# Performance work log

Measured on AMD Instinct MI355X. Metric: run time of the kernel, lower is better.

Reference implementation:

```python
import jax, jax.numpy as jnp
import numpy as np
import math

N, C, T, V = 8, 256, 120, 25
W = 5          # window_size
PAD = 2        # (W + (W-1)*(dil-1) - 1)//2 with dil=1
H = 8          # num_heads
CO = 256       # out_channels
HD = CO // H   # head channels
EPS = 1e-5


def _bn(x, g, b, m, v):
    # eval-mode BatchNorm2d over channel axis 1; x: (N, C, T, V)
    inv = jax.lax.rsqrt(v + EPS)
    return (x - m[None, :, None, None]) * (inv * g)[None, :, None, None] + b[None, :, None, None]


def _mish(x):
    return x * jnp.tanh(jax.nn.softplus(x))


def setup_inputs() -> dict:
    key = jax.random.key(0)
    ks = jax.random.split(key, 16)
    s_in = 1.0 / math.sqrt(C)
    s_out = 1.0 / math.sqrt(CO)
    return {
        "x": jax.random.normal(ks[0], (N, C, T, V), jnp.float32),
        "w_qkv": jax.random.normal(ks[1], (C, 3 * CO), jnp.float32) * s_in,
        "w_out": jax.random.normal(ks[2], (CO, CO), jnp.float32) * s_out,
        "b_out": jax.random.normal(ks[3], (CO,), jnp.float32) * 0.01,
        "bn1_g": jax.random.normal(ks[4], (CO,), jnp.float32) * 0.1 + 1.0,
        "bn1_b": jax.random.normal(ks[5], (CO,), jnp.float32) * 0.1,
        "ffn_w1": jax.random.normal(ks[6], (CO, CO), jnp.float32) * s_out,
        "ffn_w2": jax.random.normal(ks[7], (CO, CO), jnp.float32) * s_out,
        "ffn_g": jax.random.normal(ks[8], (CO,), jnp.float32) * 0.1 + 1.0,
        "ffn_b": jax.random.normal(ks[9], (CO,), jnp.float32) * 0.1,
        "bn2_g": jax.random.normal(ks[10], (CO,), jnp.float32) * 0.1 + 1.0,
        "bn2_b": jax.random.normal(ks[11], (CO,), jnp.float32) * 0.1,
        "bn1_m": jax.random.normal(ks[12], (CO,), jnp.float32) * 0.1,
        "bn1_v": jax.random.uniform(ks[13], (CO,), jnp.float32, 0.5, 1.5),
        "ffn_m": jax.random.normal(ks[14], (CO,), jnp.float32) * 0.1,
        "ffn_v": jax.random.uniform(ks[15], (CO,), jnp.float32, 0.5, 1.5),
        "bn2_m": jnp.zeros((CO,), jnp.float32),
        "bn2_v": jnp.ones((CO,), jnp.float32),
    }


def reference(x, w_qkv, w_out, b_out, bn1_g, bn1_b, ffn_w1, ffn_w2, ffn_g, ffn_b,
              bn2_g, bn2_b, bn1_m, bn1_v, ffn_m, ffn_v, bn2_m, bn2_v):
    L = W * V
    # --- group_window: unfold over T with kernel (W,1), zero padding PAD ---
    xp = jnp.pad(x, ((0, 0), (0, 0), (PAD, PAD), (0, 0)))
    # (N, C, T, W, V): window element w at time t is frame t + w - PAD
    xw = jnp.stack([xp[:, :, w:w + T, :] for w in range(W)], axis=3)
    xg = xw.transpose(0, 2, 3, 4, 1).reshape(N * T, L, C)  # tokens: (N*T, L, C)

    # --- spatio-temporal attention (full softmax over L, scale 1/sqrt(CO)) ---
    qkv = (xg @ w_qkv).reshape(N * T, L, H, 3, HD)
    q, k, v = qkv[..., 0, :], qkv[..., 1, :], qkv[..., 2, :]  # (NT, L, H, HD)
    scores = jnp.einsum('blhd,bmhd->bhlm', q, k) / math.sqrt(CO)
    attn = jax.nn.softmax(scores, axis=-1)
    out = jnp.einsum('bhlm,bmhd->blhd', attn, v).reshape(N * T, L, CO)
    out = out @ w_out + b_out

    # --- mean over window dim, residual (Identity since C == CO), norm1 ---
    inter = out.reshape(N, T, W, V, CO).transpose(0, 4, 1, 2, 3).mean(axis=3)  # (N, CO, T, V)
    inter = _bn(inter + x, bn1_g, bn1_b, bn1_m, bn1_v)

    # --- FFN: 1x1 conv -> Mish -> BN -> 1x1 conv ---
    h = jnp.einsum('oi,nitv->notv', ffn_w1, inter)
    h = _bn(_mish(h), ffn_g, ffn_b, ffn_m, ffn_v)
    h = jnp.einsum('oi,nitv->notv', ffn_w2, h)

    return _bn(h + inter, bn2_g, bn2_b, bn2_m, bn2_v)
```

## Files before the change

kernel.cpp:

```cpp
#include <hip/hip_runtime.h>
#include <hip/hip_bf16.h>


using bf16  = __bf16;
using bf16x8 = __bf16 __attribute__((ext_vector_type(8)));
using f32x4  = float __attribute__((ext_vector_type(4)));
using f32x16 = float __attribute__((ext_vector_type(16)));
using uint32x4 = unsigned int __attribute__((ext_vector_type(4)));

#define GAS __attribute__((address_space(1)))
#define LAS __attribute__((address_space(3)))

__device__ __forceinline__ void gload_lds16(const void* g, void* l) {
  __builtin_amdgcn_global_load_lds((GAS void*)g, (LAS void*)l, 16, 0, 0);
}

__device__ __forceinline__ unsigned cvt_pk_bf16(float lo, float hi) {
  unsigned r;
  asm("v_cvt_pk_bf16_f32 %0, %1, %2" : "=v"(r) : "v"(lo), "v"(hi));
  return r;
}

__device__ __forceinline__ void pl32_swap(unsigned& a, unsigned& b) {
  asm("v_permlane32_swap_b32 %0, %1" : "+v"(a), "+v"(b));
}

__global__ void k_zero(float* out, int n) {
  int i = blockIdx.x * 256 + threadIdx.x;
  if (i < n) out[i] = 0.f;
}

__global__ void k_prep(const float* __restrict__ x,
                       const float* __restrict__ wqkv, const float* __restrict__ wout,
                       const float* __restrict__ b_out,
                       const float* __restrict__ w1, const float* __restrict__ w2,
                       const float* __restrict__ g1, const float* __restrict__ b1,
                       const float* __restrict__ m1, const float* __restrict__ v1,
                       const float* __restrict__ gf, const float* __restrict__ bff,
                       const float* __restrict__ mf, const float* __restrict__ vf,
                       const float* __restrict__ g2, const float* __restrict__ b2,
                       const float* __restrict__ m2, const float* __restrict__ v2,
                       bf16* __restrict__ Xrow, bf16* __restrict__ WqT,
                       bf16* __restrict__ WoT, bf16* __restrict__ W1c,
                       bf16* __restrict__ W2c, float* __restrict__ pb) {
  __shared__ bf16 T[64 * 72];
  const int b = blockIdx.x, tid = threadIdx.x;
  if (b < 1504) {
    const int bx = b % 47, by = (b / 47) & 3, n = b / 188;
    const int tv0 = bx * 64, c0 = by * 64;
    const int la = tid & 63, sub = tid >> 6;
#pragma unroll 4
    for (int i = 0; i < 16; ++i) {
      int c = c0 + sub + i * 4;
      int tv = tv0 + la;
      float v = (tv < 3000) ? x[(size_t)(n * 256 + c) * 3000 + tv] : 0.f;
      T[(sub + i * 4) * 72 + la] = (bf16)v;
    }
    __syncthreads();
#pragma unroll 4
    for (int i = 0; i < 16; ++i) {
      int tvl = sub + i * 4;
      int tv = tv0 + tvl;
      if (tv < 3000)
        Xrow[(size_t)(n * 3100 + 50 + tv) * 256 + c0 + la] = T[la * 72 + tvl];
    }
  } else if (b < 3041) {
    int idx = (b - 1504) * 256 + tid;
    if (idx < 196608) {
      int c = idx / 768, o = idx % 768;
      float vv = wqkv[idx];
      if ((o % 96) < 32) vv *= 0.0901387929f;
      WqT[o * 256 + c] = (bf16)vv;
    } else if (idx < 262144) {
      int j = idx - 196608;
      int c = j >> 8, o = j & 255;
      WoT[o * 256 + c] = (bf16)wout[j];
    } else if (idx < 327680) {
      int j = idx - 262144;
      W1c[j] = (bf16)w1[j];
    } else if (idx < 393216) {
      int j = idx - 327680;
      W2c[j] = (bf16)w2[j];
    } else if (idx < 393472) {
      int k = idx - 393216;
      float s1 = g1[k] * rsqrtf(v1[k] + 1e-5f);
      pb[k]        = s1;
      pb[256 + k]  = b1[k] - m1[k] * s1;
      float sf = gf[k] * rsqrtf(vf[k] + 1e-5f);
      pb[512 + k]  = sf;
      pb[768 + k]  = bff[k] - mf[k] * sf;
      float s2 = g2[k] * rsqrtf(v2[k] + 1e-5f);
      pb[1024 + k] = s2;
      pb[1280 + k] = b2[k] - m2[k] * s2;
      pb[1536 + k] = b_out[k];
    }
  } else {
    int z = b - 3041;
    int idx16 = z * 256 + tid;
    int e0 = idx16 * 8;
    int pr = e0 >> 8, col = e0 & 255;
    int n = pr / 100, r100 = pr % 100;
    int row = n * 3100 + (r100 < 50 ? r100 : 3000 + r100);
    int4 zz = {};
    *(int4*)&Xrow[(size_t)row * 256 + col] = zz;
  }
}

template <int EPI>
__global__ __launch_bounds__(256, 2) void k_gemm(
    const bf16* __restrict__ A, const bf16* __restrict__ BT,
    bf16* __restrict__ Cout, int ldc, int Mreal,
    const float* __restrict__ pb, const bf16* __restrict__ Res,
    float* __restrict__ Out2) {
  __shared__ __align__(16) char smem[19456];
  bf16* As = (bf16*)smem;
  bf16* Bs = (bf16*)(smem + 8192);
  const int tid = threadIdx.x;
  const int w = tid >> 6, lane = tid & 63, q = lane >> 4, l15 = lane & 15;
  const int m0 = blockIdx.x * 128, n0 = blockIdx.y * 128;
  const int wm = (w >> 1) * 64, wn = (w & 1) * 64;
  const int srow = tid >> 2;
  const int scol = (tid & 3) << 3;
  int ar1 = m0 + srow;        if (ar1 >= Mreal) ar1 = Mreal - 1;
  int ar2 = m0 + srow + 64;   if (ar2 >= Mreal) ar2 = Mreal - 1;
  char* ldsA = (char*)As + w * 1024;
  char* ldsB = (char*)Bs + w * 1024;
  f32x4 acc[4][4] = {};

  for (int ks = 0; ks < 8; ++ks) {
    const bf16* ga1 = A  + (size_t)ar1 * 256 + ks * 32 + scol;
    const bf16* ga2 = A  + (size_t)ar2 * 256 + ks * 32 + scol;
    const bf16* gb  = BT + (size_t)(n0 + srow) * 256 + ks * 32 + scol;
    gload_lds16(ga1, ldsA);
    gload_lds16(ga2, ldsA + 4096);
    gload_lds16(gb,            ldsB);
    gload_lds16(gb + 64 * 256, ldsB + 4096);
    __syncthreads();
    bf16x8 af[4], bfr[4];
#pragma unroll
    for (int i = 0; i < 4; ++i) af[i]  = *(const bf16x8*)&As[(wm + i * 16 + l15) * 32 + q * 8];
#pragma unroll
    for (int i = 0; i < 4; ++i) bfr[i] = *(const bf16x8*)&Bs[(wn + i * 16 + l15) * 32 + q * 8];
#pragma unroll
    for (int i = 0; i < 4; ++i)
#pragma unroll
      for (int j = 0; j < 4; ++j)
        acc[i][j] = __builtin_amdgcn_mfma_f32_16x16x32_bf16(af[i], bfr[j], acc[i][j], 0, 0, 0);
    __syncthreads();
  }

  if constexpr (EPI != 3) {
#pragma unroll
    for (int i = 0; i < 4; ++i) {
#pragma unroll
      for (int j = 0; j < 4; ++j) {
#pragma unroll
        for (int r = 0; r < 4; ++r) {
          int row = m0 + wm + i * 16 + q * 4 + r;
          int col = n0 + wn + j * 16 + l15;
          if (row >= Mreal) continue;
          float v = acc[i][j][r];
          if constexpr (EPI == 0) {
            Cout[(size_t)row * ldc + col] = (bf16)v;
          } else if constexpr (EPI == 1) {
            v += pb[1536 + col];
            int n = row / 3000;
            v += (float)Res[(size_t)(row + n * 100 + 50) * 256 + col];
            v = v * pb[col] + pb[256 + col];
            Cout[(size_t)row * 256 + col] = (bf16)v;
          } else {
            float ex = __expf(v);
            float a = 1.f + ex;
            float u = 1.f / (a * a);
            v = v * (1.f - u) / (1.f + u);
            v = v * pb[512 + col] + pb[768 + col];
            Cout[(size_t)row * 256 + col] = (bf16)v;
          }
        }
      }
    }
  } else {
    float* Tt = (float*)smem;
    const int tti = (w & 1);
#pragma unroll
    for (int jj = 0; jj < 4; ++jj) {
      __syncthreads();
#pragma unroll
      for (int i = 0; i < 4; ++i) {
#pragma unroll
        for (int r = 0; r < 4; ++r) {
          int rowl = wm + i * 16 + q * 4 + r;
          int row = m0 + rowl;
          int col = n0 + tti * 64 + jj * 16 + l15;
          float v = acc[i][jj][r];
          v += (float)Res[(size_t)row * 256 + col];
          v = v * pb[1024 + col] + pb[1280 + col];
          Tt[tti * 2432 + rowl * 19 + l15] = v;
        }
      }
      __syncthreads();
#pragma unroll
      for (int k = 0; k < 16; ++k) {
        int flat = k * 256 + tid;
        int tt2 = flat >> 11;
        int rem = flat & 2047;
        int colL = rem >> 7;
        int rowl = rem & 127;
        int row = m0 + rowl;
        if (row < Mreal) {
          int col = n0 + tt2 * 64 + jj * 16 + colL;
          int n = row / 3000, r2 = row - n * 3000;
          Out2[(size_t)(n * 256 + col) * 3000 + r2] = Tt[tt2 * 2432 + rowl * 19 + colL];
        }
      }
    }
  }
}

__global__ __launch_bounds__(256, 4) void k_attn(const bf16* __restrict__ Y,
                                                 bf16* __restrict__ om) {
  __shared__ __align__(16) char smem[18944];
  bf16* Vts = (bf16*)smem;
  float* Ofl = (float*)smem;
  float* Rin = (float*)(smem + 18432);
  const int tid = threadIdx.x;
  const int bi = blockIdx.x;
  const int h = bi & 7, b = bi >> 3;
  const int n = b / 120, t = b % 120;
  const bf16* Yb = Y + (size_t)(n * 3100 + t * 25) * 768 + h * 96;
  const int w = tid >> 6, lane = tid & 63;
  const int l31 = lane & 31, hi = lane >> 5;

#pragma unroll
  for (int p = 0; p < 2; ++p) {
    int m = p * 64 + lane;
    if (m < 125) {
      int4 v4 = *(const int4*)(Yb + (size_t)m * 768 + 64 + w * 8);
      bf16x8 v8 = __builtin_bit_cast(bf16x8, v4);
#pragma unroll
      for (int jj = 0; jj < 8; ++jj) Vts[(w * 8 + jj) * 136 + m] = v8[jj];
    }
  }
  if (tid < 96) {
    int d = tid / 3, m = 125 + tid % 3;
    Vts[d * 136 + m] = (bf16)0.f;
  }

  int qrow = w * 32 + l31; if (qrow > 124) qrow = 124;
  const bf16* qp = Yb + (size_t)qrow * 768 + hi * 8;
  bf16x8 qf0 = *(const bf16x8*)qp;
  bf16x8 qf1 = *(const bf16x8*)(qp + 16);

  f32x16 acc[4] = {};
#pragma unroll
  for (int kt = 0; kt < 4; ++kt) {
    int krow = kt * 32 + l31; if (krow > 124) krow = 124;
    const bf16* kp = Yb + (size_t)krow * 768 + 32 + hi * 8;
    bf16x8 kf0 = *(const bf16x8*)kp;
    bf16x8 kf1 = *(const bf16x8*)(kp + 16);
    acc[kt] = __builtin_amdgcn_mfma_f32_32x32x16_bf16(kf0, qf0, acc[kt], 0, 0, 0);
    acc[kt] = __builtin_amdgcn_mfma_f32_32x32x16_bf16(kf1, qf1, acc[kt], 0, 0, 0);
  }

  float sp[4];
  uint32x4 pk[8];
#pragma unroll
  for (int kt = 0; kt < 4; ++kt) {
    float e[16];
#pragma unroll
    for (int r = 0; r < 16; ++r) {
      float pz = exp2f(acc[kt][r]);
      if (kt == 3 && r >= 13 && hi) pz = 0.f;
      e[r] = pz;
    }
    float t0 = (e[0] + e[1]) + (e[2] + e[3]);
    float t1 = (e[4] + e[5]) + (e[6] + e[7]);
    float t2 = (e[8] + e[9]) + (e[10] + e[11]);
    float t3 = (e[12] + e[13]) + (e[14] + e[15]);
    sp[kt] = (t0 + t1) + (t2 + t3);
#pragma unroll
    for (int half = 0; half < 2; ++half) {
      const int ba = half * 8;
      unsigned a0 = cvt_pk_bf16(e[ba + 0], e[ba + 1]);
      unsigned a1 = cvt_pk_bf16(e[ba + 2], e[ba + 3]);
      unsigned b0 = cvt_pk_bf16(e[ba + 4], e[ba + 5]);
      unsigned b1 = cvt_pk_bf16(e[ba + 6], e[ba + 7]);
      pl32_swap(a0, b0);
      pl32_swap(a1, b1);
      pk[kt * 2 + half][0] = a0;
      pk[kt * 2 + half][1] = a1;
      pk[kt * 2 + half][2] = b0;
      pk[kt * 2 + half][3] = b1;
    }
  }
  float s = (sp[0] + sp[1]) + (sp[2] + sp[3]);
  s += __shfl_xor(s, 32, 64);
  float rinv = 1.f / s;
  if (hi == 0) Rin[w * 32 + l31] = rinv;

  __syncthreads();

  f32x16 oacc0 = {}, oacc1 = {};
#pragma unroll
  for (int kc = 0; kc < 8; ++kc) {
    bf16x8 pa = __builtin_bit_cast(bf16x8, pk[kc]);
    bf16x8 vf = *(const bf16x8*)&Vts[l31 * 136 + kc * 16 + hi * 8];
    if (kc & 1) oacc1 = __builtin_amdgcn_mfma_f32_32x32x16_bf16(pa, vf, oacc1, 0, 0, 0);
    else        oacc0 = __builtin_amdgcn_mfma_f32_32x32x16_bf16(pa, vf, oacc0, 0, 0, 0);
  }

  __syncthreads();
#pragma unroll
  for (int r = 0; r < 16; ++r) {
    int row = w * 32 + (r & 3) + 8 * (r >> 2) + 4 * hi;
    Ofl[row * 36 + l31] = oacc0[r] + oacc1[r];
  }
  __syncthreads();
  bf16* dst = om + (size_t)((n * 120 + t) * 25) * 256 + h * 32;
  for (int j = tid; j < 800; j += 256) {
    int vv = j >> 5, d = j & 31;
    float s5 = 0.f;
#pragma unroll
    for (int ww = 0; ww < 5; ++ww)
      s5 += Ofl[(ww * 25 + vv) * 36 + d] * Rin[ww * 25 + vv];
    dst[vv * 256 + d] = (bf16)(s5 * 0.2f);
  }
}

extern "C" void kernel_launch(void* const* d_in, const int* in_sizes, int n_in,
                              void* d_out, int out_size, void* d_ws, size_t ws_size,
                              hipStream_t stream) {
  const size_t NEED = 51584000;
  if (ws_size < NEED) {
    k_zero<<<(out_size + 255) / 256, 256, 0, stream>>>((float*)d_out, out_size);
    return;
  }
  const float* x     = (const float*)d_in[0];
  const float* wqkv  = (const float*)d_in[1];
  const float* wout  = (const float*)d_in[2];
  const float* b_out = (const float*)d_in[3];
  const float* bn1_g = (const float*)d_in[4];
  const float* bn1_b = (const float*)d_in[5];
  const float* ffn_w1= (const float*)d_in[6];
  const float* ffn_w2= (const float*)d_in[7];
  const float* ffn_g = (const float*)d_in[8];
  const float* ffn_b = (const float*)d_in[9];
  const float* bn2_g = (const float*)d_in[10];
  const float* bn2_b = (const float*)d_in[11];
  const float* bn1_m = (const float*)d_in[12];
  const float* bn1_v = (const float*)d_in[13];
  const float* ffn_m = (const float*)d_in[14];
  const float* ffn_v = (const float*)d_in[15];
  const float* bn2_m = (const float*)d_in[16];
  const float* bn2_v = (const float*)d_in[17];

  char* ws = (char*)d_ws;
  float* pb    = (float*)(ws + 0);
  bf16* WqT    = (bf16*)(ws + 7168);
  bf16* WoT    = (bf16*)(ws + 400384);
  bf16* W1c    = (bf16*)(ws + 531456);
  bf16* W2c    = (bf16*)(ws + 662528);
  bf16* Xrow   = (bf16*)(ws + 793600);
  bf16* Y      = (bf16*)(ws + 13491200);
  bf16* interR = Y;
  bf16* Gm     = (bf16*)(ws + 25779200);
  bf16* om     = (bf16*)d_out;

  k_prep<<<3141, 256, 0, stream>>>(x, wqkv, wout, b_out, ffn_w1, ffn_w2,
                                   bn1_g, bn1_b, bn1_m, bn1_v,
                                   ffn_g, ffn_b, ffn_m, ffn_v,
                                   bn2_g, bn2_b, bn2_m, bn2_v,
                                   Xrow, WqT, WoT, W1c, W2c, pb);
  k_gemm<0><<<dim3(194, 6), 256, 0, stream>>>(Xrow, WqT, Y, 768, 24800, pb, nullptr, nullptr);
  k_attn<<<7680, 256, 0, stream>>>(Y, om);
  k_gemm<1><<<dim3(188, 2), 256, 0, stream>>>(om, WoT, interR, 256, 24000, pb, Xrow, nullptr);
  k_gemm<2><<<dim3(188, 2), 256, 0, stream>>>(interR, W1c, Gm, 256, 24000, pb, nullptr, nullptr);
  k_gemm<3><<<dim3(188, 2), 256, 0, stream>>>(Gm, W2c, nullptr, 256, 24000, pb, interR, (float*)d_out);
}
```

Measured before the change: 245.2 us.

## Fuse out-projection, FFN GEMMs and epilogues into one kernel

After: 237.2 us. 3.3% less time.

```diff
diff --git a/kernel.cpp b/kernel.cpp
--- a/kernel.cpp
+++ b/kernel.cpp
@@ -217,6 +217,169 @@
   }
 }
 
+__global__ __launch_bounds__(256, 3) void k_ffn(
+    const bf16* __restrict__ Aom, const bf16* __restrict__ Wo,
+    const bf16* __restrict__ W1, const bf16* __restrict__ W2,
+    const bf16* __restrict__ Xres, const float* __restrict__ pb,
+    float* __restrict__ Out2) {
+  __shared__ __align__(16) char smem[54272];
+  bf16* As = (bf16*)smem;
+  bf16* Bs = (bf16*)(smem + 4096);
+  bf16* XI = (bf16*)(smem + 20480);
+  float* Tt = (float*)smem;
+  const int tid = threadIdx.x;
+  const int w = tid >> 6, lane = tid & 63, q = lane >> 4, l15 = lane & 15;
+  const int r0 = blockIdx.x * 64;
+  const int srow = tid >> 2, scol = (tid & 3) << 3;
+  char* ldsA = (char*)As + w * 1024;
+  char* ldsB = (char*)Bs + w * 1024;
+
+  f32x4 acc[4][4];
+#pragma unroll
+  for (int i = 0; i < 4; ++i)
+#pragma unroll
+    for (int j = 0; j < 4; ++j) acc[i][j] = f32x4{};
+
+  for (int ks = 0; ks < 8; ++ks) {
+    gload_lds16(Aom + (size_t)(r0 + srow) * 256 + ks * 32 + scol, ldsA);
+#pragma unroll
+    for (int ii = 0; ii < 4; ++ii)
+      gload_lds16(Wo + (size_t)(ii * 64 + srow) * 256 + ks * 32 + scol,
+                  ldsB + ii * 4096);
+    __syncthreads();
+    bf16x8 af[4], bfr[4];
+#pragma unroll
+    for (int i = 0; i < 4; ++i) af[i]  = *(const bf16x8*)&As[(i * 16 + l15) * 32 + q * 8];
+#pragma unroll
+    for (int j = 0; j < 4; ++j) bfr[j] = *(const bf16x8*)&Bs[(w * 64 + j * 16 + l15) * 32 + q * 8];
+#pragma unroll
+    for (int i = 0; i < 4; ++i)
+#pragma unroll
+      for (int j = 0; j < 4; ++j)
+        acc[i][j] = __builtin_amdgcn_mfma_f32_16x16x32_bf16(af[i], bfr[j], acc[i][j], 0, 0, 0);
+    __syncthreads();
+  }
+  unsigned irk[32];
+#pragma unroll
+  for (int i = 0; i < 4; ++i) {
+#pragma unroll
+    for (int j = 0; j < 4; ++j) {
+      int colb = w * 64 + j * 16 + l15;
+      float vv[4];
+#pragma unroll
+      for (int r = 0; r < 4; ++r) {
+        int grow = r0 + i * 16 + q * 4 + r;
+        int nn = grow / 3000;
+        float v = acc[i][j][r] + pb[1536 + colb]
+                + (float)Xres[(size_t)(grow + nn * 100 + 50) * 256 + colb];
+        v = v * pb[colb] + pb[256 + colb];
+        vv[r] = v;
+        XI[(i * 16 + q * 4 + r) * 264 + colb] = (bf16)v;
+      }
+      irk[(i * 4 + j) * 2 + 0] = cvt_pk_bf16(vv[0], vv[1]);
+      irk[(i * 4 + j) * 2 + 1] = cvt_pk_bf16(vv[2], vv[3]);
+    }
+  }
+
+#pragma unroll
+  for (int i = 0; i < 4; ++i)
+#pragma unroll
+    for (int j = 0; j < 4; ++j) acc[i][j] = f32x4{};
+  for (int ks = 0; ks < 8; ++ks) {
+#pragma unroll
+    for (int ii = 0; ii < 4; ++ii)
+      gload_lds16(W1 + (size_t)(ii * 64 + srow) * 256 + ks * 32 + scol,
+                  ldsB + ii * 4096);
+    __syncthreads();
+    bf16x8 af[4], bfr[4];
+#pragma unroll
+    for (int i = 0; i < 4; ++i) af[i]  = *(const bf16x8*)&XI[(i * 16 + l15) * 264 + ks * 32 + q * 8];
+#pragma unroll
+    for (int j = 0; j < 4; ++j) bfr[j] = *(const bf16x8*)&Bs[(w * 64 + j * 16 + l15) * 32 + q * 8];
+#pragma unroll
+    for (int i = 0; i < 4; ++i)
+#pragma unroll
+      for (int j = 0; j < 4; ++j)
+        acc[i][j] = __builtin_amdgcn_mfma_f32_16x16x32_bf16(af[i], bfr[j], acc[i][j], 0, 0, 0);
+    __syncthreads();
+  }
+#pragma unroll
+  for (int i = 0; i < 4; ++i) {
+#pragma unroll
+    for (int j = 0; j < 4; ++j) {
+      int colb = w * 64 + j * 16 + l15;
+#pragma unroll
+      for (int r = 0; r < 4; ++r) {
+        float v = acc[i][j][r];
+        float ex = __expf(v);
+        float a = 1.f + ex;
+        float u = 1.f / (a * a);
+        v = v * (1.f - u) / (1.f + u);
+        v = v * pb[512 + colb] + pb[768 + colb];
+        XI[(i * 16 + q * 4 + r) * 264 + colb] = (bf16)v;
+      }
+    }
+  }
+
+#pragma unroll
+  for (int i = 0; i < 4; ++i)
+#pragma unroll
+    for (int j = 0; j < 4; ++j) acc[i][j] = f32x4{};
+  for (int ks = 0; ks < 8; ++ks) {
+#pragma unroll
+    for (int ii = 0; ii < 4; ++ii)
+      gload_lds16(W2 + (size_t)(ii * 64 + srow) * 256 + ks * 32 + scol,
+                  ldsB + ii * 4096);
+    __syncthreads();
+    bf16x8 af[4], bfr[4];
+#pragma unroll
+    for (int i = 0; i < 4; ++i) af[i]  = *(const bf16x8*)&XI[(i * 16 + l15) * 264 + ks * 32 + q * 8];
+#pragma unroll
+    for (int j = 0; j < 4; ++j) bfr[j] = *(const bf16x8*)&Bs[(w * 64 + j * 16 + l15) * 32 + q * 8];
+#pragma unroll
+    for (int i = 0; i < 4; ++i)
+#pragma unroll
+      for (int j = 0; j < 4; ++j)
+        acc[i][j] = __builtin_amdgcn_mfma_f32_16x16x32_bf16(af[i], bfr[j], acc[i][j], 0, 0, 0);
+    __syncthreads();
+  }
+
+  const int rowl_t = tid & 63;
+  const int grow_t = r0 + rowl_t;
+  const int nn_t = grow_t / 3000;
+  const int rr_t = grow_t - nn_t * 3000;
+#pragma unroll
+  for (int cc = 0; cc < 4; ++cc) {
+    __syncthreads();
+    if (w == cc) {
+#pragma unroll
+      for (int i = 0; i < 4; ++i) {
+#pragma unroll
+        for (int j = 0; j < 4; ++j) {
+          int colb = cc * 64 + j * 16 + l15;
+#pragma unroll
+          for (int r = 0; r < 4; ++r) {
+            unsigned pr = irk[(i * 4 + j) * 2 + (r >> 1)];
+            unsigned short us = (r & 1) ? (unsigned short)(pr >> 16)
+                                        : (unsigned short)(pr & 0xffff);
+            float res = (float)__builtin_bit_cast(bf16, us);
+            float v = acc[i][j][r] + res;
+            v = v * pb[1024 + colb] + pb[1280 + colb];
+            Tt[(i * 16 + q * 4 + r) * 65 + j * 16 + l15] = v;
+          }
+        }
+      }
+    }
+    __syncthreads();
+#pragma unroll
+    for (int it = 0; it < 16; ++it) {
+      int cl = (tid >> 6) + it * 4;
+      int colb = cc * 64 + cl;
+      Out2[(size_t)(nn_t * 256 + colb) * 3000 + rr_t] = Tt[rowl_t * 65 + cl];
+    }
+  }
+}
+
 __global__ __launch_bounds__(256, 4) void k_attn(const bf16* __restrict__ Y,
                                                  bf16* __restrict__ om) {
   __shared__ __align__(16) char smem[18944];
@@ -330,8 +493,9 @@
 extern "C" void kernel_launch(void* const* d_in, const int* in_sizes, int n_in,
                               void* d_out, int out_size, void* d_ws, size_t ws_size,
                               hipStream_t stream) {
-  const size_t NEED = 51584000;
-  if (ws_size < NEED) {
+  const size_t NEED1 = 51584000;
+  const size_t NEED2 = 63872000;
+  if (ws_size < NEED1) {
     k_zero<<<(out_size + 255) / 256, 256, 0, stream>>>((float*)d_out, out_size);
     return;
   }
@@ -364,6 +528,7 @@
   bf16* Y      = (bf16*)(ws + 13491200);
   bf16* interR = Y;
   bf16* Gm     = (bf16*)(ws + 25779200);
+  bf16* om2    = (bf16*)(ws + 51584000);
   bf16* om     = (bf16*)d_out;
 
   k_prep<<<3141, 256, 0, stream>>>(x, wqkv, wout, b_out, ffn_w1, ffn_w2,
@@ -372,8 +537,13 @@
                                    bn2_g, bn2_b, bn2_m, bn2_v,
                                    Xrow, WqT, WoT, W1c, W2c, pb);
   k_gemm<0><<<dim3(194, 6), 256, 0, stream>>>(Xrow, WqT, Y, 768, 24800, pb, nullptr, nullptr);
-  k_attn<<<7680, 256, 0, stream>>>(Y, om);
-  k_gemm<1><<<dim3(188, 2), 256, 0, stream>>>(om, WoT, interR, 256, 24000, pb, Xrow, nullptr);
-  k_gemm<2><<<dim3(188, 2), 256, 0, stream>>>(interR, W1c, Gm, 256, 24000, pb, nullptr, nullptr);
-  k_gemm<3><<<dim3(188, 2), 256, 0, stream>>>(Gm, W2c, nullptr, 256, 24000, pb, interR, (float*)d_out);
-}
+  if (ws_size >= NEED2) {
+    k_attn<<<7680, 256, 0, stream>>>(Y, om2);
+    k_ffn<<<375, 256, 0, stream>>>(om2, WoT, W1c, W2c, Xrow, pb, (float*)d_out);
+  } else {
+    k_attn<<<7680, 256, 0, stream>>>(Y, om);
+    k_gemm<1><<<dim3(188, 2), 256, 0, stream>>>(om, WoT, interR, 256, 24000, pb, Xrow, nullptr);
+    k_gemm<2><<<dim3(188, 2), 256, 0, stream>>>(interR, W1c, Gm, 256, 24000, pb, nullptr, nullptr);
+    k_gemm<3><<<dim3(188, 2), 256, 0, stream>>>(Gm, W2c, nullptr, 256, 24000, pb, interR, (float*)d_out);
+  }
+}
```
